# Performance work log

Hardware: AMD Instinct MI355X
Metric: run time of the kernel (lower is better)

## Reference

```python
import jax, jax.numpy as jnp
import numpy as np

EMBED = 2560
HEADS = 8
HEAD_DIM = EMBED // HEADS

def setup_inputs() -> dict:
    key = jax.random.key(0)
    k1, k2, k3, k4, k5 = jax.random.split(key, 5)
    x = jax.random.normal(k1, (2, 2048, EMBED), dtype=jnp.float32)
    # nn.Linear(embed, 3*embed): weight [3E, E], bias [3E]
    s = 1.0 / np.sqrt(EMBED)
    W_qkv = jax.random.uniform(k2, (3 * EMBED, EMBED), jnp.float32, -s, s)
    b_qkv = jax.random.uniform(k3, (3 * EMBED,), jnp.float32, -s, s)
    W_out = jax.random.uniform(k4, (EMBED, EMBED), jnp.float32, -s, s)
    b_out = jax.random.uniform(k5, (EMBED,), jnp.float32, -s, s)
    return {"x": x, "W_qkv": W_qkv, "b_qkv": b_qkv, "W_out": W_out, "b_out": b_out}

def reference(x, W_qkv, b_qkv, W_out, b_out):
    N, S, E = x.shape
    qkv = jnp.einsum('bse,fe->bsf', x, W_qkv) + b_qkv            # [B,S,3E]
    qkv = qkv.reshape(N, S, 3, HEADS, HEAD_DIM)
    q = jnp.transpose(qkv[:, :, 0], (0, 2, 1, 3))                 # [B,H,S,D]
    k = jnp.transpose(qkv[:, :, 1], (0, 2, 1, 3))
    v = jnp.transpose(qkv[:, :, 2], (0, 2, 1, 3))
    scale = jnp.sqrt(jnp.float32(HEAD_DIM))
    attn = jnp.einsum('bhqd,bhkd->bhqk', q, k) / scale            # [B,H,S,S]
    attn = jax.nn.softmax(attn, axis=-1)
    out = jnp.einsum('bhqk,bhkd->bhqd', attn, v)                  # [B,H,S,D]
    out = jnp.transpose(out, (0, 2, 1, 3)).reshape(N, S, E)
    return jnp.einsum('bse,fe->bsf', out, W_out) + b_out
```

## Files before the change

kernel.cpp:

```cpp
#include <hip/hip_runtime.h>

#define EMBED 2560
#define HEADS 8
#define HDIM  320
#define BATCH 2
#define SEQ   2048
#define MTOT  (BATCH*SEQ)
#define FTOT  (3*EMBED)

using bf = __bf16;
typedef __bf16 bf16x8 __attribute__((ext_vector_type(8)));
typedef float  f32x4  __attribute__((ext_vector_type(4)));
typedef short  s16x8  __attribute__((ext_vector_type(8)));
typedef float  f32x4v __attribute__((ext_vector_type(4)));

__device__ __forceinline__ void gl_lds16(const bf* g, bf* l) {
    __builtin_amdgcn_global_load_lds(
        (const __attribute__((address_space(1))) void*)g,
        (__attribute__((address_space(3))) void*)l,
        16, 0, 0);
}

__global__ void cvt_bf16(const float* __restrict__ in, bf* __restrict__ out, int n) {
    int i = (blockIdx.x*blockDim.x + threadIdx.x)*8;
    if (i >= n) return;
    f32x4v a = *reinterpret_cast<const f32x4v*>(in + i);
    f32x4v b = *reinterpret_cast<const f32x4v*>(in + i + 4);
    bf16x8 r;
    r[0]=(bf)a[0]; r[1]=(bf)a[1]; r[2]=(bf)a[2]; r[3]=(bf)a[3];
    r[4]=(bf)b[0]; r[5]=(bf)b[1]; r[6]=(bf)b[2]; r[7]=(bf)b[3];
    *reinterpret_cast<bf16x8*>(out + i) = r;
}

template<bool OUTBF>
__global__ __launch_bounds__(512, 2)
void gemm256(const bf* __restrict__ A, const bf* __restrict__ B,
             const float* __restrict__ bias, void* __restrict__ Cp,
             int M, int N, int K) {
    __shared__ __align__(16) bf AsL[2][2][8192];
    __shared__ __align__(16) bf BsL[2][2][8192];
    const int tid = threadIdx.x, lane = tid & 63, wid = tid >> 6;
    const int wr = wid >> 2, wc = wid & 3;
    const int l15 = lane & 15, l4 = lane >> 4;

    const int nwg = gridDim.x*gridDim.y;
    int bid = blockIdx.y*gridDim.x + blockIdx.x;
    if ((nwg & 7) == 0) bid = (bid & 7)*(nwg >> 3) + (bid >> 3);
    const int m0 = (bid / gridDim.x)*256, n0 = (bid % gridDim.x)*256;
    const int NT = K >> 6;

    unsigned aOff[2];
    #pragma unroll
    for (int j = 0; j < 2; ++j) {
        int q = (wid*2 + j)*64 + lane;
        int r = q >> 3, c = q & 7;
        aOff[j] = (unsigned)r*K + (unsigned)((c ^ (r & 7))*8);
    }
    const bf* Ap = A + (size_t)m0*K;
    const bf* Bp = B + (size_t)n0*K;

    auto stA = [&](int bb, int h, int kt) {
        bf* d = &AsL[bb][h][wid*1024];
        const bf* s = Ap + (size_t)h*128*K + (size_t)kt*64;
        gl_lds16(s + aOff[0], d);
        gl_lds16(s + aOff[1], d + 512);
    };
    auto stB = [&](int bb, int h, int kt) {
        bf* d = &BsL[bb][h][wid*1024];
        const bf* s = Bp + (size_t)h*128*K + (size_t)kt*64;
        gl_lds16(s + aOff[0], d);
        gl_lds16(s + aOff[1], d + 512);
    };

    f32x4 acc[8][4] = {};
    bf16x8 aR[4][2], bR0[2][2], bR1[2][2];

    stB(0,0,0); stB(0,1,0); stA(0,0,0); stA(0,1,0); stB(1,0,1); stB(1,1,1);
    asm volatile("s_waitcnt vmcnt(4)" ::: "memory");
    __builtin_amdgcn_s_barrier();

    const int brow0 = (wc & 1)*64;
    for (int kt = 0; kt < NT; ++kt) {
        const int bb = kt & 1;
        const bf* Ab = &AsL[bb][wr][0];
        const bf* Bb = &BsL[bb][wc >> 1][0];

        #pragma unroll
        for (int mi = 0; mi < 4; ++mi)
            #pragma unroll
            for (int kk = 0; kk < 2; ++kk) {
                int r = mi*16 + l15;
                int kg = kk*4 + l4;
                aR[mi][kk] = *reinterpret_cast<const bf16x8*>(&Ab[r*64 + ((kg ^ (r & 7))*8)]);
            }
        #pragma unroll
        for (int ni = 0; ni < 2; ++ni)
            #pragma unroll
            for (int kk = 0; kk < 2; ++kk) {
                int r = brow0 + ni*16 + l15;
                int kg = kk*4 + l4;
                bR0[ni][kk] = *reinterpret_cast<const bf16x8*>(&Bb[r*64 + ((kg ^ (r & 7))*8)]);
            }
        if (kt + 1 < NT) stA(bb^1, 0, kt+1);
        __builtin_amdgcn_s_barrier();
        __builtin_amdgcn_s_setprio(1);
        #pragma unroll
        for (int mi = 0; mi < 4; ++mi)
            #pragma unroll
            for (int ni = 0; ni < 2; ++ni)
                #pragma unroll
                for (int kk = 0; kk < 2; ++kk)
                    acc[mi][ni] = __builtin_amdgcn_mfma_f32_16x16x32_bf16(aR[mi][kk], bR0[ni][kk], acc[mi][ni], 0, 0, 0);
        __builtin_amdgcn_s_setprio(0);
        __builtin_amdgcn_s_barrier();

        #pragma unroll
        for (int ni = 0; ni < 2; ++ni)
            #pragma unroll
            for (int kk = 0; kk < 2; ++kk) {
                int r = brow0 + 32 + ni*16 + l15;
                int kg = kk*4 + l4;
                bR1[ni][kk] = *reinterpret_cast<const bf16x8*>(&Bb[r*64 + ((kg ^ (r & 7))*8)]);
            }
        if (kt + 1 < NT) stA(bb^1, 1, kt+1);
        __builtin_amdgcn_s_barrier();
        __builtin_amdgcn_s_setprio(1);
        #pragma unroll
        for (int mi = 0; mi < 4; ++mi)
            #pragma unroll
            for (int ni = 0; ni < 2; ++ni)
                #pragma unroll
                for (int kk = 0; kk < 2; ++kk)
                    acc[mi][2+ni] = __builtin_amdgcn_mfma_f32_16x16x32_bf16(aR[mi][kk], bR1[ni][kk], acc[mi][2+ni], 0, 0, 0);
        __builtin_amdgcn_s_setprio(0);
        __builtin_amdgcn_s_barrier();

        #pragma unroll
        for (int mi = 0; mi < 4; ++mi)
            #pragma unroll
            for (int kk = 0; kk < 2; ++kk) {
                int r = 64 + mi*16 + l15;
                int kg = kk*4 + l4;
                aR[mi][kk] = *reinterpret_cast<const bf16x8*>(&Ab[r*64 + ((kg ^ (r & 7))*8)]);
            }
        if (kt + 2 < NT) stB(bb, 0, kt+2);
        __builtin_amdgcn_s_barrier();
        __builtin_amdgcn_s_setprio(1);
        #pragma unroll
        for (int mi = 0; mi < 4; ++mi)
            #pragma unroll
            for (int ni = 0; ni < 2; ++ni)
                #pragma unroll
                for (int kk = 0; kk < 2; ++kk)
                    acc[4+mi][2+ni] = __builtin_amdgcn_mfma_f32_16x16x32_bf16(aR[mi][kk], bR1[ni][kk], acc[4+mi][2+ni], 0, 0, 0);
        __builtin_amdgcn_s_setprio(0);
        __builtin_amdgcn_s_barrier();

        if (kt + 2 < NT) stB(bb, 1, kt+2);
        if (kt >= NT-2) asm volatile("s_waitcnt vmcnt(0)" ::: "memory");
        else            asm volatile("s_waitcnt vmcnt(4)" ::: "memory");
        __builtin_amdgcn_s_barrier();
        __builtin_amdgcn_s_setprio(1);
        #pragma unroll
        for (int mi = 0; mi < 4; ++mi)
            #pragma unroll
            for (int ni = 0; ni < 2; ++ni)
                #pragma unroll
                for (int kk = 0; kk < 2; ++kk)
                    acc[4+mi][ni] = __builtin_amdgcn_mfma_f32_16x16x32_bf16(aR[mi][kk], bR0[ni][kk], acc[4+mi][ni], 0, 0, 0);
        __builtin_amdgcn_s_setprio(0);
        __builtin_amdgcn_s_barrier();
    }

    const int cr0 = m0 + wr*128, cc0 = n0 + wc*64;
    #pragma unroll
    for (int NI = 0; NI < 4; ++NI) {
        int colg = cc0 + NI*16 + l15;
        float bv = bias[colg];
        #pragma unroll
        for (int MI = 0; MI < 8; ++MI)
            #pragma unroll
            for (int rr = 0; rr < 4; ++rr) {
                int rowg = cr0 + MI*16 + l4*4 + rr;
                float v = acc[MI][NI][rr] + bv;
                if (OUTBF) ((bf*)Cp)[(size_t)rowg*N + colg] = (bf)v;
                else       ((float*)Cp)[(size_t)rowg*N + colg] = v;
            }
    }
}

__global__ void repack_vt(const bf* __restrict__ qkv, bf* __restrict__ vt) {
    __shared__ bf tile[64][72];
    const int bh = blockIdx.z, b = bh >> 3, h = bh & 7;
    const int s0 = blockIdx.x*64, d0 = blockIdx.y*64;
    const int t = threadIdx.x;
    #pragma unroll
    for (int p = 0; p < 2; ++p) {
        int sr = (t >> 3) + p*32, ck = t & 7;
        s16x8 v = *reinterpret_cast<const s16x8*>(
            qkv + ((size_t)(b*SEQ + s0 + sr))*FTOT + 2*EMBED + h*HDIM + d0 + ck*8);
        *reinterpret_cast<s16x8*>(&tile[sr][ck*8]) = v;
    }
    __syncthreads();
    #pragma unroll
    for (int p = 0; p < 2; ++p) {
        int dr = (t >> 3) + p*32, ck = t & 7;
        bf16x8 r;
        #pragma unroll
        for (int j = 0; j < 8; ++j) r[j] = tile[ck*8 + j][dr];
        *reinterpret_cast<bf16x8*>(vt + ((size_t)bh*HDIM + d0 + dr)*SEQ + s0 + ck*8) = r;
    }
}

__global__ __launch_bounds__(512, 2)
void attn_fwd(const bf* __restrict__ qkv, const bf* __restrict__ vt, bf* __restrict__ aout) {
    __shared__ bf Kls[2][32*320];
    __shared__ bf Vls[2][320*32];
    __shared__ bf Ps[8][16][40];
    const int bh = blockIdx.y, b = bh >> 3, h = bh & 7;
    const int tid = threadIdx.x, lane = tid & 63, wid = tid >> 6;
    const int qw = blockIdx.x*128 + wid*16;
    const int l15 = lane & 15, l4 = lane >> 4;
    const float scale = 0.05590169944f;

    const bf* gsrc[5];
    int ldsoff[5];
    size_t step;
    if (wid < 4) {
        step = (size_t)32*FTOT;
        #pragma unroll
        for (int i = 0; i < 5; ++i) {
            int g = wid*5 + i;
            int q = g*64 + lane;
            int r = q/40, cl = q - r*40;
            int cg = cl ^ (r & 7);
            gsrc[i] = qkv + (size_t)(b*SEQ + r)*FTOT + EMBED + h*HDIM + cg*8;
            ldsoff[i] = g*512;
        }
    } else {
        step = 32;
        #pragma unroll
        for (int i = 0; i < 5; ++i) {
            int g = wid*5 + i - 20;
            int q = g*64 + lane;
            int row = q >> 2, cl = q & 3;
            int cg = cl ^ ((row >> 1) & 3);
            gsrc[i] = vt + (size_t)bh*HDIM*SEQ + (size_t)row*SEQ + cg*8;
            ldsoff[i] = g*512;
        }
    }

    bf16x8 qf[10];
    const bf* qbase = qkv + ((size_t)(b*SEQ + qw + l15))*FTOT + h*HDIM + l4*8;
    #pragma unroll
    for (int d = 0; d < 10; ++d) qf[d] = *reinterpret_cast<const bf16x8*>(qbase + d*32);

    f32x4 o[20] = {};
    float mrow[4], lsum[4];
    #pragma unroll
    for (int r = 0; r < 4; ++r) { mrow[r] = -1e30f; lsum[r] = 0.f; }

    const int r7  = l15 & 7;
    const int vsw = (l4 ^ ((l15 >> 1) & 3))*8;

    {
        bf* lb = (wid < 4) ? &Kls[0][0] : &Vls[0][0];
        #pragma unroll
        for (int i = 0; i < 5; ++i) { gl_lds16(gsrc[i], lb + ldsoff[i]); gsrc[i] += step; }
    }
    __syncthreads();

    for (int kt = 0; kt < SEQ/32; ++kt) {
        const int bb = kt & 1;
        if (kt + 1 < SEQ/32) {
            bf* lb = (wid < 4) ? &Kls[bb^1][0] : &Vls[bb^1][0];
            #pragma unroll
            for (int i = 0; i < 5; ++i) { gl_lds16(gsrc[i], lb + ldsoff[i]); gsrc[i] += step; }
        }
        const bf* Kb = &Kls[bb][0];
        const bf* Vb = &Vls[bb][0];

        f32x4 sc[2] = {};
        #pragma unroll
        for (int kb = 0; kb < 2; ++kb) {
            const int Rbase = (kb*16 + l15)*320;
            #pragma unroll
            for (int d = 0; d < 10; ++d) {
                int c = (d*4 + l4) ^ r7;
                bf16x8 kf = *reinterpret_cast<const bf16x8*>(&Kb[Rbase + c*8]);
                sc[kb] = __builtin_amdgcn_mfma_f32_16x16x32_bf16(qf[d], kf, sc[kb], 0, 0, 0);
            }
        }

        float tmax[4];
        bool need = false;
        #pragma unroll
        for (int r = 0; r < 4; ++r) {
            float v = fmaxf(sc[0][r], sc[1][r])*scale;
            v = fmaxf(v, __shfl_xor(v, 1));
            v = fmaxf(v, __shfl_xor(v, 2));
            v = fmaxf(v, __shfl_xor(v, 4));
            v = fmaxf(v, __shfl_xor(v, 8));
            tmax[r] = v;
            need = need || (v > mrow[r] + 8.f);
        }
        if (__any(need)) {
            float alpha[4];
            #pragma unroll
            for (int r = 0; r < 4; ++r) {
                float nm = fmaxf(mrow[r], tmax[r]);
                alpha[r] = __expf(mrow[r] - nm);
                mrow[r] = nm;
                lsum[r] *= alpha[r];
            }
            #pragma unroll
            for (int c = 0; c < 20; ++c)
                #pragma unroll
                for (int r = 0; r < 4; ++r) o[c][r] *= alpha[r];
        }

        float ps[2][4];
        #pragma unroll
        for (int r = 0; r < 4; ++r) {
            float p0 = __expf(sc[0][r]*scale - mrow[r]);
            float p1 = __expf(sc[1][r]*scale - mrow[r]);
            ps[0][r] = p0; ps[1][r] = p1;
            lsum[r] += p0 + p1;
        }

        #pragma unroll
        for (int kb = 0; kb < 2; ++kb)
            #pragma unroll
            for (int r = 0; r < 4; ++r)
                Ps[wid][l4*4 + r][kb*16 + l15] = (bf)ps[kb][r];

        bf16x8 pf = *reinterpret_cast<const bf16x8*>(&Ps[wid][l15][l4*8]);
        #pragma unroll
        for (int c = 0; c < 20; ++c) {
            bf16x8 vf = *reinterpret_cast<const bf16x8*>(&Vb[(c*16 + l15)*32 + vsw]);
            o[c] = __builtin_amdgcn_mfma_f32_16x16x32_bf16(pf, vf, o[c], 0, 0, 0);
        }
        __syncthreads();
    }

    float inv[4];
    #pragma unroll
    for (int r = 0; r < 4; ++r) {
        float s = lsum[r];
        s += __shfl_xor(s, 1);
        s += __shfl_xor(s, 2);
        s += __shfl_xor(s, 4);
        s += __shfl_xor(s, 8);
        inv[r] = 1.f/s;
    }
    #pragma unroll
    for (int c = 0; c < 20; ++c)
        #pragma unroll
        for (int r = 0; r < 4; ++r) {
            size_t idx = ((size_t)(b*SEQ + qw + l4*4 + r))*EMBED + h*HDIM + c*16 + l15;
            aout[idx] = (bf)(o[c][r]*inv[r]);
        }
}

extern "C" void kernel_launch(void* const* d_in, const int* in_sizes, int n_in,
                              void* d_out, int out_size, void* d_ws, size_t ws_size,
                              hipStream_t stream) {
    const float* x    = (const float*)d_in[0];
    const float* Wqkv = (const float*)d_in[1];
    const float* bqkv = (const float*)d_in[2];
    const float* Wout = (const float*)d_in[3];
    const float* bout = (const float*)d_in[4];
    float* out = (float*)d_out;

    char* ws = (char*)d_ws;
    bf* xb    = (bf*)(ws);
    bf* wqkvb = (bf*)(ws + 20971520);
    bf* woutb = (bf*)(ws + 60293120);
    bf* qkvb  = (bf*)(ws + 73400320);
    bf* vtb   = (bf*)(ws + 136314880);
    bf* attnb = xb;

    cvt_bf16<<<5120, 256, 0, stream>>>(x,    xb,    MTOT*EMBED);
    cvt_bf16<<<9600, 256, 0, stream>>>(Wqkv, wqkvb, FTOT*EMBED);
    cvt_bf16<<<3200, 256, 0, stream>>>(Wout, woutb, EMBED*EMBED);

    gemm256<true ><<<dim3(FTOT/256,  MTOT/256), 512, 0, stream>>>(xb, wqkvb, bqkv, qkvb, MTOT, FTOT, EMBED);
    repack_vt<<<dim3(SEQ/64, HDIM/64, BATCH*HEADS), 256, 0, stream>>>(qkvb, vtb);
    attn_fwd<<<dim3(SEQ/128, BATCH*HEADS), 512, 0, stream>>>(qkvb, vtb, attnb);
    gemm256<false><<<dim3(EMBED/256, MTOT/256), 512, 0, stream>>>(attnb, woutb, bout, out, MTOT, EMBED, EMBED);
}
```

Measured before the change: 417.2 us.

## Prefetch next-iteration LDS fragments into separate registers in the GEMM main loop

The GEMM inner loop now keeps separate low and high register fragments for both A and B. Next-iteration A and B fragments are read from the other LDS buffer during the last MFMA phase of the current iteration, so LDS read latency overlaps with matrix math instead of stalling before each phase. A sched_barrier and an explicit lgkmcnt wait pin the ordering. In exchange, register pressure rises, which could reduce occupancy or cause spills. Reading from the alternate buffer also relies on the existing vmcnt and barrier placement to avoid races.

```diff
diff --git a/kernel.cpp b/kernel.cpp
--- a/kernel.cpp
+++ b/kernel.cpp
@@ -73,34 +73,44 @@
     };
 
     f32x4 acc[8][4] = {};
-    bf16x8 aR[4][2], bR0[2][2], bR1[2][2];
+    bf16x8 aLo[4][2], aHi[4][2], bLo[2][2], bHi[2][2];
+    const int brow0 = (wc & 1)*64;
+
+    auto rdA = [&](bf16x8 (&dst)[4][2], const bf* Ab, int rbase) {
+        #pragma unroll
+        for (int mi = 0; mi < 4; ++mi)
+            #pragma unroll
+            for (int kk = 0; kk < 2; ++kk) {
+                int r = rbase + mi*16 + l15;
+                int kg = kk*4 + l4;
+                dst[mi][kk] = *reinterpret_cast<const bf16x8*>(&Ab[r*64 + ((kg ^ (r & 7))*8)]);
+            }
+    };
+    auto rdB = [&](bf16x8 (&dst)[2][2], const bf* Bb, int rbase) {
+        #pragma unroll
+        for (int ni = 0; ni < 2; ++ni)
+            #pragma unroll
+            for (int kk = 0; kk < 2; ++kk) {
+                int r = rbase + ni*16 + l15;
+                int kg = kk*4 + l4;
+                dst[ni][kk] = *reinterpret_cast<const bf16x8*>(&Bb[r*64 + ((kg ^ (r & 7))*8)]);
+            }
+    };
 
     stB(0,0,0); stB(0,1,0); stA(0,0,0); stA(0,1,0); stB(1,0,1); stB(1,1,1);
     asm volatile("s_waitcnt vmcnt(4)" ::: "memory");
     __builtin_amdgcn_s_barrier();
-
-    const int brow0 = (wc & 1)*64;
+    rdA(aLo, &AsL[0][wr][0], 0);
+    rdB(bLo, &BsL[0][wc >> 1][0], brow0);
+
     for (int kt = 0; kt < NT; ++kt) {
         const int bb = kt & 1;
-        const bf* Ab = &AsL[bb][wr][0];
-        const bf* Bb = &BsL[bb][wc >> 1][0];
-
-        #pragma unroll
-        for (int mi = 0; mi < 4; ++mi)
-            #pragma unroll
-            for (int kk = 0; kk < 2; ++kk) {
-                int r = mi*16 + l15;
-                int kg = kk*4 + l4;
-                aR[mi][kk] = *reinterpret_cast<const bf16x8*>(&Ab[r*64 + ((kg ^ (r & 7))*8)]);
-            }
-        #pragma unroll
-        for (int ni = 0; ni < 2; ++ni)
-            #pragma unroll
-            for (int kk = 0; kk < 2; ++kk) {
-                int r = brow0 + ni*16 + l15;
-                int kg = kk*4 + l4;
-                bR0[ni][kk] = *reinterpret_cast<const bf16x8*>(&Bb[r*64 + ((kg ^ (r & 7))*8)]);
-            }
+        const bf* Ab  = &AsL[bb][wr][0];
+        const bf* Bb  = &BsL[bb][wc >> 1][0];
+        const bf* AbN = &AsL[bb^1][wr][0];
+        const bf* BbN = &BsL[bb^1][wc >> 1][0];
+
+        rdB(bHi, Bb, brow0 + 32);
         if (kt + 1 < NT) stA(bb^1, 0, kt+1);
         __builtin_amdgcn_s_barrier();
         __builtin_amdgcn_s_setprio(1);
@@ -110,18 +120,11 @@
             for (int ni = 0; ni < 2; ++ni)
                 #pragma unroll
                 for (int kk = 0; kk < 2; ++kk)
-                    acc[mi][ni] = __builtin_amdgcn_mfma_f32_16x16x32_bf16(aR[mi][kk], bR0[ni][kk], acc[mi][ni], 0, 0, 0);
+                    acc[mi][ni] = __builtin_amdgcn_mfma_f32_16x16x32_bf16(aLo[mi][kk], bLo[ni][kk], acc[mi][ni], 0, 0, 0);
         __builtin_amdgcn_s_setprio(0);
         __builtin_amdgcn_s_barrier();
 
-        #pragma unroll
-        for (int ni = 0; ni < 2; ++ni)
-            #pragma unroll
-            for (int kk = 0; kk < 2; ++kk) {
-                int r = brow0 + 32 + ni*16 + l15;
-                int kg = kk*4 + l4;
-                bR1[ni][kk] = *reinterpret_cast<const bf16x8*>(&Bb[r*64 + ((kg ^ (r & 7))*8)]);
-            }
+        rdA(aHi, Ab, 64);
         if (kt + 1 < NT) stA(bb^1, 1, kt+1);
         __builtin_amdgcn_s_barrier();
         __builtin_amdgcn_s_setprio(1);
@@ -131,18 +134,10 @@
             for (int ni = 0; ni < 2; ++ni)
                 #pragma unroll
                 for (int kk = 0; kk < 2; ++kk)
-                    acc[mi][2+ni] = __builtin_amdgcn_mfma_f32_16x16x32_bf16(aR[mi][kk], bR1[ni][kk], acc[mi][2+ni], 0, 0, 0);
+                    acc[mi][2+ni] = __builtin_amdgcn_mfma_f32_16x16x32_bf16(aLo[mi][kk], bHi[ni][kk], acc[mi][2+ni], 0, 0, 0);
         __builtin_amdgcn_s_setprio(0);
         __builtin_amdgcn_s_barrier();
 
-        #pragma unroll
-        for (int mi = 0; mi < 4; ++mi)
-            #pragma unroll
-            for (int kk = 0; kk < 2; ++kk) {
-                int r = 64 + mi*16 + l15;
-                int kg = kk*4 + l4;
-                aR[mi][kk] = *reinterpret_cast<const bf16x8*>(&Ab[r*64 + ((kg ^ (r & 7))*8)]);
-            }
         if (kt + 2 < NT) stB(bb, 0, kt+2);
         __builtin_amdgcn_s_barrier();
         __builtin_amdgcn_s_setprio(1);
@@ -152,7 +147,7 @@
             for (int ni = 0; ni < 2; ++ni)
                 #pragma unroll
                 for (int kk = 0; kk < 2; ++kk)
-                    acc[4+mi][2+ni] = __builtin_amdgcn_mfma_f32_16x16x32_bf16(aR[mi][kk], bR1[ni][kk], acc[4+mi][2+ni], 0, 0, 0);
+                    acc[4+mi][2+ni] = __builtin_amdgcn_mfma_f32_16x16x32_bf16(aHi[mi][kk], bHi[ni][kk], acc[4+mi][2+ni], 0, 0, 0);
         __builtin_amdgcn_s_setprio(0);
         __builtin_amdgcn_s_barrier();
 
@@ -160,6 +155,8 @@
         if (kt >= NT-2) asm volatile("s_waitcnt vmcnt(0)" ::: "memory");
         else            asm volatile("s_waitcnt vmcnt(4)" ::: "memory");
         __builtin_amdgcn_s_barrier();
+        if (kt + 1 < NT) rdA(aLo, AbN, 0);
+        __builtin_amdgcn_sched_barrier(0);
         __builtin_amdgcn_s_setprio(1);
         #pragma unroll
         for (int mi = 0; mi < 4; ++mi)
@@ -167,8 +164,10 @@
             for (int ni = 0; ni < 2; ++ni)
                 #pragma unroll
                 for (int kk = 0; kk < 2; ++kk)
-                    acc[4+mi][ni] = __builtin_amdgcn_mfma_f32_16x16x32_bf16(aR[mi][kk], bR0[ni][kk], acc[4+mi][ni], 0, 0, 0);
+                    acc[4+mi][ni] = __builtin_amdgcn_mfma_f32_16x16x32_bf16(aHi[mi][kk], bLo[ni][kk], acc[4+mi][ni], 0, 0, 0);
         __builtin_amdgcn_s_setprio(0);
+        if (kt + 1 < NT) rdB(bLo, BbN, brow0);
+        asm volatile("s_waitcnt lgkmcnt(0)" ::: "memory");
         __builtin_amdgcn_s_barrier();
     }
 
```

Result: slower. 484.7 us (+16.2%).
